# Kernel tuning notes

Hardware: AMD Instinct MI355X
Metric: run time of the kernel (lower is better)

The kernel has to match this reference:

```python
import jax, jax.numpy as jnp
import numpy as np

N = 50000        # nodes
E = 1_600_000    # edges
F_IN = 128       # in_channels
H = 128          # hidden_dim (== F_IN so GCN weights stack)
L = 3            # num_layers
LSTM_H = 256     # lstm_hidden
OUT = 32         # output_dim
G = 64           # number of graphs in the batch


def setup_inputs() -> dict:
    key = jax.random.key(0)
    ks = jax.random.split(key, 8)
    x = jax.random.normal(ks[0], (N, F_IN), dtype=jnp.float32)
    edge_index = jax.random.randint(ks[1], (2, E), 0, N, dtype=jnp.int32)
    batch = jnp.sort(jax.random.randint(ks[2], (N,), 0, G, dtype=jnp.int32))
    # GCN layer weights (all [H,H] since F_IN == H), PyG-style glorot scale
    Wg = jax.random.normal(ks[3], (L, F_IN, H), dtype=jnp.float32) / np.sqrt(F_IN)
    bg = jnp.zeros((L, H), dtype=jnp.float32)
    # torch LSTM params, gate order (i, f, g, o)
    W_ih = jax.random.normal(ks[4], (4 * LSTM_H, H), dtype=jnp.float32) / np.sqrt(H)
    W_hh = jax.random.normal(ks[5], (4 * LSTM_H, LSTM_H), dtype=jnp.float32) / np.sqrt(LSTM_H)
    b_ih = jnp.zeros((4 * LSTM_H,), dtype=jnp.float32)
    b_hh = jnp.zeros((4 * LSTM_H,), dtype=jnp.float32)
    W_out = jax.random.normal(ks[6], (OUT, LSTM_H), dtype=jnp.float32) / np.sqrt(LSTM_H)
    b_out = jnp.zeros((OUT,), dtype=jnp.float32)
    return dict(x=x, edge_index=edge_index, batch=batch, Wg=Wg, bg=bg,
                W_ih=W_ih, W_hh=W_hh, b_ih=b_ih, b_hh=b_hh,
                W_out=W_out, b_out=b_out)


def reference(x, edge_index, batch, Wg, bg, W_ih, W_hh, b_ih, b_hh, W_out, b_out):
    n = x.shape[0]
    # PyG GCNConv gcn_norm: add self-loops, symmetric D^{-1/2}(A+I)D^{-1/2}
    loop = jnp.arange(n, dtype=edge_index.dtype)
    row = jnp.concatenate([edge_index[0], loop])  # source nodes (x_j)
    col = jnp.concatenate([edge_index[1], loop])  # target nodes (aggregate here)
    deg = jax.ops.segment_sum(jnp.ones_like(col, dtype=x.dtype), col, num_segments=n)
    dinv = jnp.where(deg > 0, jax.lax.rsqrt(deg), 0.0)
    norm = (dinv[row] * dinv[col])[:, None]  # [E+N, 1]

    h = x
    for l in range(Wg.shape[0]):
        t = h @ Wg[l]                                     # [N, H] transform first
        msg = t[row] * norm                               # gather + scale  [E+N, H]
        agg = jax.ops.segment_sum(msg, col, num_segments=n)  # scatter-add  [N, H]
        h = jax.nn.relu(agg + bg[l])

    # global_mean_pool over batch segment ids
    cnt = jax.ops.segment_sum(jnp.ones((n,), h.dtype), batch, num_segments=G)
    pooled = jax.ops.segment_sum(h, batch, num_segments=G) / jnp.maximum(cnt, 1.0)[:, None]  # [G, H]

    # single-step LSTM with zero initial state (seq_len = 1)
    h0 = jnp.zeros((G, W_hh.shape[1]), pooled.dtype)
    gates = pooled @ W_ih.T + h0 @ W_hh.T + b_ih + b_hh   # [G, 4*LSTM_H]
    i, f, g, o = jnp.split(gates, 4, axis=-1)             # torch gate order i,f,g,o
    c = jax.nn.sigmoid(i) * jnp.tanh(g)                   # c0 = 0 => forget term drops
    hn = jax.nn.sigmoid(o) * jnp.tanh(c)                  # [G, LSTM_H]

    return hn @ W_out.T + b_out                            # [G, OUT]
```

## Files before the change

### kernel.cpp

```cpp
#include <hip/hip_runtime.h>

constexpr int NN = 50000;
constexpr int NE = 1600000;
constexpr int H  = 128;
constexpr int LH = 256;
constexpr int OD = 32;
constexpr int NG = 64;

constexpr int NBKT  = (NN + 255) / 256;
constexpr int PARTE = 4096;
constexpr int NPARTB = (NE + PARTE - 1) / PARTE;
static_assert(NBKT <= 256, "single-block scan assumes NBKT <= 256");

constexpr int BCH = 4;
constexpr int BCW = 32;

constexpr int LSZ = 4608;

typedef __attribute__((ext_vector_type(8))) short short8v;
typedef __attribute__((ext_vector_type(4))) float f32x4;

union BF8 { uint4 u; short8v s; };

__device__ __forceinline__ unsigned short f2bf(float x) {
    unsigned int u = __float_as_uint(x);
    u = (u + 0x7FFFu + ((u >> 16) & 1u)) >> 16;
    return (unsigned short)u;
}

__global__ __launch_bounds__(256) void k_bhist(const int* __restrict__ col,
                                               int* __restrict__ bktCnt) {
    __shared__ int h[NBKT];
    int t = threadIdx.x;
    if (t < NBKT) h[t] = 0;
    __syncthreads();
    for (int i = blockIdx.x * 256 + t; i < NE; i += gridDim.x * 256)
        atomicAdd(&h[col[i] >> 8], 1);
    __syncthreads();
    if (t < NBKT && h[t] > 0) atomicAdd(&bktCnt[t], h[t]);
}

__global__ __launch_bounds__(256) void k_bscan(const int* __restrict__ bktCnt,
                                               int* __restrict__ bktBase,
                                               int* __restrict__ bktCursor) {
    __shared__ int sh[256];
    int t = threadIdx.x;
    int v = (t < NBKT) ? bktCnt[t] : 0;
    sh[t] = v;
    __syncthreads();
    for (int off = 1; off < 256; off <<= 1) {
        int add = (t >= off) ? sh[t - off] : 0;
        __syncthreads();
        sh[t] += add;
        __syncthreads();
    }
    if (t < NBKT) {
        int excl = sh[t] - v;
        bktBase[t] = excl;
        bktCursor[t] = excl;
    }
    if (t == NBKT - 1) bktBase[NBKT] = sh[t];
}

__global__ __launch_bounds__(256) void k_part(const int* __restrict__ ei,
                                              int* __restrict__ bktCursor,
                                              int* __restrict__ part) {
    __shared__ int lcur[NBKT];
    __shared__ int lbase[NBKT];
    const int t = threadIdx.x;
    const int base = blockIdx.x * PARTE;
    int pk[16], bk[16];

    if (t < NBKT) lcur[t] = 0;
    __syncthreads();
#pragma unroll
    for (int j = 0; j < 16; ++j) {
        int e = base + j * 256 + t;
        if (e < NE) {
            int sr = ei[e];
            int ds = ei[NE + e];
            pk[j] = (sr << 8) | (ds & 255);
            bk[j] = ds >> 8;
            atomicAdd(&lcur[bk[j]], 1);
        }
    }
    __syncthreads();
    if (t < NBKT) {
        int c = lcur[t];
        lbase[t] = (c > 0) ? atomicAdd(&bktCursor[t], c) : 0;
        lcur[t] = 0;
    }
    __syncthreads();
#pragma unroll
    for (int j = 0; j < 16; ++j) {
        int e = base + j * 256 + t;
        if (e < NE) {
            int r = atomicAdd(&lcur[bk[j]], 1);
            part[lbase[bk[j]] + r] = pk[j];
        }
    }
}

__global__ __launch_bounds__(256) void k_bfill(const int* __restrict__ bktBase,
                                               const int* __restrict__ part,
                                               int* __restrict__ rp,
                                               int* __restrict__ cnt,
                                               float* __restrict__ dinv,
                                               int* __restrict__ srcs) {
    __shared__ int h[256];
    __shared__ int sc[256];
    __shared__ int cur[256];
    const int b = blockIdx.x, t = threadIdx.x;
    const int lo = bktBase[b], hi = bktBase[b + 1];

    h[t] = 0;
    __syncthreads();
    for (int i = lo + t; i < hi; i += 256)
        atomicAdd(&h[part[i] & 255], 1);
    __syncthreads();
    int v = h[t];
    sc[t] = v;
    __syncthreads();
    for (int off = 1; off < 256; off <<= 1) {
        int add = (t >= off) ? sc[t - off] : 0;
        __syncthreads();
        sc[t] += add;
        __syncthreads();
    }
    int excl = sc[t] - v;
    cur[t] = lo + excl;
    int node = b * 256 + t;
    if (node < NN) {
        rp[node] = lo + excl;
        cnt[node] = v;
        dinv[node] = rsqrtf((float)v + 1.0f);
    }
    __syncthreads();
    for (int i = lo + t; i < hi; i += 256) {
        int e = part[i];
        int pos = atomicAdd(&cur[e & 255], 1);
        srcs[pos] = e >> 8;
    }
}

template <bool RELU, bool CHIN>
__global__ __launch_bounds__(256) void k_gemm(const float* __restrict__ hf,
                                              const unsigned short* __restrict__ hb,
                                              const float* __restrict__ W,
                                              const float* __restrict__ dinv,
                                              unsigned short* __restrict__ tb) {
    __shared__ uint4 lw[2048];
    const int tid = threadIdx.x;

    for (int e = tid; e < 2048; e += 256) {
        const int ct = e >> 8, ks = (e >> 6) & 3, l = e & 63;
        const int col = ct * 16 + (l & 15);
        const int kb  = ks * 32 + ((l >> 4) << 3);
        const float* wp = W + (size_t)kb * H + col;
        unsigned int p0 = (unsigned)f2bf(wp[0])     | ((unsigned)f2bf(wp[H])     << 16);
        unsigned int p1 = (unsigned)f2bf(wp[2 * H]) | ((unsigned)f2bf(wp[3 * H]) << 16);
        unsigned int p2 = (unsigned)f2bf(wp[4 * H]) | ((unsigned)f2bf(wp[5 * H]) << 16);
        unsigned int p3 = (unsigned)f2bf(wp[6 * H]) | ((unsigned)f2bf(wp[7 * H]) << 16);
        lw[e] = make_uint4(p0, p1, p2, p3);
    }
    __syncthreads();

    const int wave = tid >> 6, lane = tid & 63;
    const int rowbase = blockIdx.x * 64 + wave * 16;
    const int arow  = rowbase + (lane & 15);
    const int arowc = arow < NN ? arow : NN - 1;
    const int koff  = (lane >> 4) << 3;

    f32x4 acc[8];
#pragma unroll
    for (int ct = 0; ct < 8; ++ct) acc[ct] = (f32x4){0.f, 0.f, 0.f, 0.f};

#pragma unroll
    for (int ks = 0; ks < 4; ++ks) {
        BF8 a;
        if (CHIN) {
            a.u = *reinterpret_cast<const uint4*>(
                hb + ((size_t)ks * NN + arowc) * BCW + koff);
            if (RELU) {
                unsigned int m;
                m = ((a.u.x >> 15) & 0x00010001u) * 0xFFFFu; a.u.x &= ~m;
                m = ((a.u.y >> 15) & 0x00010001u) * 0xFFFFu; a.u.y &= ~m;
                m = ((a.u.z >> 15) & 0x00010001u) * 0xFFFFu; a.u.z &= ~m;
                m = ((a.u.w >> 15) & 0x00010001u) * 0xFFFFu; a.u.w &= ~m;
            }
        } else {
            const int kb = ks * 32 + koff;
            const float* base = hf + (size_t)arowc * H + kb;
            float4 h0 = *reinterpret_cast<const float4*>(base);
            float4 h1 = *reinterpret_cast<const float4*>(base + 4);
            if (RELU) {
                h0.x = fmaxf(h0.x, 0.f); h0.y = fmaxf(h0.y, 0.f);
                h0.z = fmaxf(h0.z, 0.f); h0.w = fmaxf(h0.w, 0.f);
                h1.x = fmaxf(h1.x, 0.f); h1.y = fmaxf(h1.y, 0.f);
                h1.z = fmaxf(h1.z, 0.f); h1.w = fmaxf(h1.w, 0.f);
            }
            a.u = make_uint4(
                (unsigned)f2bf(h0.x) | ((unsigned)f2bf(h0.y) << 16),
                (unsigned)f2bf(h0.z) | ((unsigned)f2bf(h0.w) << 16),
                (unsigned)f2bf(h1.x) | ((unsigned)f2bf(h1.y) << 16),
                (unsigned)f2bf(h1.z) | ((unsigned)f2bf(h1.w) << 16));
        }
#pragma unroll
        for (int ct = 0; ct < 8; ++ct) {
            BF8 b;
            b.u = lw[(ct * 4 + ks) * 64 + lane];
            acc[ct] = __builtin_amdgcn_mfma_f32_16x16x32_bf16(a.s, b.s, acc[ct], 0, 0, 0);
        }
    }

    const int colb = lane & 15;
    const int rrow = rowbase + ((lane >> 4) << 2);
#pragma unroll
    for (int r = 0; r < 4; ++r) {
        const int row = rrow + r;
        if (row < NN) {
            const float d = dinv[row];
#pragma unroll
            for (int ct = 0; ct < 8; ++ct) {
                const int feat = ct * 16 + colb;
                tb[((size_t)(feat >> 5) * NN + row) * BCW + (feat & 31)] =
                    f2bf(acc[ct][r] * d);
            }
        }
    }
}

template <int POOL>
__global__ __launch_bounds__(256) void k_gather(const int* __restrict__ rp,
                                                const int* __restrict__ cnt,
                                                const int* __restrict__ srcs,
                                                const float* __restrict__ dinv,
                                                const float* __restrict__ bg,
                                                const unsigned short* __restrict__ tb,
                                                unsigned short* __restrict__ aggb,
                                                const int* __restrict__ batch,
                                                float* __restrict__ pooled) {
    __shared__ int lsrcs[LSZ];
    const int tid  = threadIdx.x;
    const int wv   = tid >> 6;
    const int lane = tid & 63;
    const int slot = lane >> 2;
    const int l4   = lane & 3;
    const int c    = blockIdx.x & 3;
    const int nb   = blockIdx.x >> 2;
    const int n0   = nb * 64;
    const int n    = n0 + wv * 16 + slot;

    const int eLo = rp[n0];
    int nLast = n0 + 63; if (nLast >= NN) nLast = NN - 1;
    const int eHi = rp[nLast] + cnt[nLast];
    const bool staged = (eHi - eLo) <= LSZ;

    if (staged) {
        for (int i = eLo + tid; i < eHi; i += 256)
            lsrcs[i - eLo] = srcs[i];
    }

    __shared__ float psum[4][32];
    int g0 = 0, gspan = 0;
    if (POOL) {
        if (tid < 128) psum[tid >> 5][tid & 31] = 0.f;
        g0 = batch[n0];
        gspan = batch[nLast] - g0;
    }
    __syncthreads();

    if (n >= NN) return;

    const uint4* __restrict__ tb4 =
        reinterpret_cast<const uint4*>(tb) + (size_t)c * NN * 4;
    const float4 bg0 = *reinterpret_cast<const float4*>(bg + c * BCW + l4 * 8);
    const float4 bg1 = *reinterpret_cast<const float4*>(bg + c * BCW + l4 * 8 + 4);

    const int i0  = rp[n];
    const int end = i0 + cnt[n];
    float4 p = make_float4(0.f, 0.f, 0.f, 0.f);
    float4 q = make_float4(0.f, 0.f, 0.f, 0.f);

#define ACC8(v)                                                        \
    do {                                                               \
        p.x += __uint_as_float((v).x << 16);                           \
        p.y += __uint_as_float((v).x & 0xFFFF0000u);                   \
        p.z += __uint_as_float((v).y << 16);                           \
        p.w += __uint_as_float((v).y & 0xFFFF0000u);                   \
        q.x += __uint_as_float((v).z << 16);                           \
        q.y += __uint_as_float((v).z & 0xFFFF0000u);                   \
        q.z += __uint_as_float((v).w << 16);                           \
        q.w += __uint_as_float((v).w & 0xFFFF0000u);                   \
    } while (0)

    if (staged) {
        int i = i0;
        for (; i + 7 < end; i += 8) {
            int s0 = lsrcs[i     - eLo], s1 = lsrcs[i + 1 - eLo];
            int s2 = lsrcs[i + 2 - eLo], s3 = lsrcs[i + 3 - eLo];
            int s4 = lsrcs[i + 4 - eLo], s5 = lsrcs[i + 5 - eLo];
            int s6 = lsrcs[i + 6 - eLo], s7 = lsrcs[i + 7 - eLo];
            uint4 v0 = tb4[(size_t)s0 * 4 + l4];
            uint4 v1 = tb4[(size_t)s1 * 4 + l4];
            uint4 v2 = tb4[(size_t)s2 * 4 + l4];
            uint4 v3 = tb4[(size_t)s3 * 4 + l4];
            uint4 v4 = tb4[(size_t)s4 * 4 + l4];
            uint4 v5 = tb4[(size_t)s5 * 4 + l4];
            uint4 v6 = tb4[(size_t)s6 * 4 + l4];
            uint4 v7 = tb4[(size_t)s7 * 4 + l4];
            ACC8(v0); ACC8(v1); ACC8(v2); ACC8(v3);
            ACC8(v4); ACC8(v5); ACC8(v6); ACC8(v7);
        }
        for (; i < end; ++i) {
            uint4 v = tb4[(size_t)lsrcs[i - eLo] * 4 + l4];
            ACC8(v);
        }
    } else {
        int i = i0;
        for (; i + 3 < end; i += 4) {
            int s0 = srcs[i], s1 = srcs[i + 1], s2 = srcs[i + 2], s3 = srcs[i + 3];
            uint4 v0 = tb4[(size_t)s0 * 4 + l4];
            uint4 v1 = tb4[(size_t)s1 * 4 + l4];
            uint4 v2 = tb4[(size_t)s2 * 4 + l4];
            uint4 v3 = tb4[(size_t)s3 * 4 + l4];
            ACC8(v0); ACC8(v1); ACC8(v2); ACC8(v3);
        }
        for (; i < end; ++i) {
            uint4 v = tb4[(size_t)srcs[i] * 4 + l4];
            ACC8(v);
        }
    }

    uint4 sv = tb4[(size_t)n * 4 + l4];
    ACC8(sv);
#undef ACC8

    const float d = dinv[n];
    float4 o0, o1;
    o0.x = fmaf(p.x, d, bg0.x); o0.y = fmaf(p.y, d, bg0.y);
    o0.z = fmaf(p.z, d, bg0.z); o0.w = fmaf(p.w, d, bg0.w);
    o1.x = fmaf(q.x, d, bg1.x); o1.y = fmaf(q.y, d, bg1.y);
    o1.z = fmaf(q.z, d, bg1.z); o1.w = fmaf(q.w, d, bg1.w);

    if (POOL == 0) {
        uint4 u;
        u.x = (unsigned)f2bf(o0.x) | ((unsigned)f2bf(o0.y) << 16);
        u.y = (unsigned)f2bf(o0.z) | ((unsigned)f2bf(o0.w) << 16);
        u.z = (unsigned)f2bf(o1.x) | ((unsigned)f2bf(o1.y) << 16);
        u.w = (unsigned)f2bf(o1.z) | ((unsigned)f2bf(o1.w) << 16);
        *reinterpret_cast<uint4*>(aggb + ((size_t)c * NN + n) * BCW + l4 * 8) = u;
    } else {
        o0.x = fmaxf(o0.x, 0.f); o0.y = fmaxf(o0.y, 0.f);
        o0.z = fmaxf(o0.z, 0.f); o0.w = fmaxf(o0.w, 0.f);
        o1.x = fmaxf(o1.x, 0.f); o1.y = fmaxf(o1.y, 0.f);
        o1.z = fmaxf(o1.z, 0.f); o1.w = fmaxf(o1.w, 0.f);
        if (gspan > 3) {
            float* dst = pooled + (size_t)batch[n] * H + c * BCW + l4 * 8;
            atomicAdd(dst + 0, o0.x); atomicAdd(dst + 1, o0.y);
            atomicAdd(dst + 2, o0.z); atomicAdd(dst + 3, o0.w);
            atomicAdd(dst + 4, o1.x); atomicAdd(dst + 5, o1.y);
            atomicAdd(dst + 6, o1.z); atomicAdd(dst + 7, o1.w);
        } else if (gspan == 0) {
#pragma unroll
            for (int m = 4; m <= 32; m <<= 1) {
                o0.x += __shfl_xor(o0.x, m); o0.y += __shfl_xor(o0.y, m);
                o0.z += __shfl_xor(o0.z, m); o0.w += __shfl_xor(o0.w, m);
                o1.x += __shfl_xor(o1.x, m); o1.y += __shfl_xor(o1.y, m);
                o1.z += __shfl_xor(o1.z, m); o1.w += __shfl_xor(o1.w, m);
            }
            if (slot == 0) {
                float* ps = &psum[wv][l4 * 8];
                ps[0] = o0.x; ps[1] = o0.y; ps[2] = o0.z; ps[3] = o0.w;
                ps[4] = o1.x; ps[5] = o1.y; ps[6] = o1.z; ps[7] = o1.w;
            }
            __syncthreads();
            if (tid < 32) {
                float v = psum[0][tid] + psum[1][tid] + psum[2][tid] + psum[3][tid];
                atomicAdd(&pooled[(size_t)g0 * H + c * BCW + tid], v);
            }
        } else {
            const int gi = batch[n] - g0;
            float* ps = &psum[gi][l4 * 8];
            atomicAdd(ps + 0, o0.x); atomicAdd(ps + 1, o0.y);
            atomicAdd(ps + 2, o0.z); atomicAdd(ps + 3, o0.w);
            atomicAdd(ps + 4, o1.x); atomicAdd(ps + 5, o1.y);
            atomicAdd(ps + 6, o1.z); atomicAdd(ps + 7, o1.w);
            __syncthreads();
            if (tid < 128) {
                int gi2 = tid >> 5, f = tid & 31;
                float v = psum[gi2][f];
                if (v != 0.f)
                    atomicAdd(&pooled[(size_t)(g0 + gi2) * H + c * BCW + f], v);
            }
        }
    }
}

__device__ __forceinline__ int lower_bound_dev(const int* __restrict__ b, int v) {
    int lo = 0, hi = NN;
    while (lo < hi) {
        int m = (lo + hi) >> 1;
        if (b[m] < v) lo = m + 1; else hi = m;
    }
    return lo;
}

__global__ __launch_bounds__(256) void k_lstm(const float* __restrict__ pooled,
                                              const int* __restrict__ batch,
                                              const float* __restrict__ W_ih,
                                              const float* __restrict__ b_ih,
                                              const float* __restrict__ b_hh,
                                              const float* __restrict__ W_out,
                                              const float* __restrict__ b_out,
                                              float* __restrict__ out) {
    __shared__ __align__(16) float p[H];
    __shared__ __align__(16) float hn[LH];
    int g = blockIdx.x, t = threadIdx.x;
    if (t < H) {
        int s = lower_bound_dev(batch, g);
        int e = lower_bound_dev(batch, g + 1);
        p[t] = pooled[g * H + t] / fmaxf((float)(e - s), 1.f);
    }
    __syncthreads();

    float si = b_ih[t] + b_hh[t];
    float sg = b_ih[2 * LH + t] + b_hh[2 * LH + t];
    float so = b_ih[3 * LH + t] + b_hh[3 * LH + t];
    const float* wi = W_ih + (size_t)t * H;
    const float* wg = W_ih + (size_t)(2 * LH + t) * H;
    const float* wo = W_ih + (size_t)(3 * LH + t) * H;
    for (int k = 0; k < H; k += 4) {
        float4 pv = *reinterpret_cast<const float4*>(&p[k]);
        float4 a = *reinterpret_cast<const float4*>(wi + k);
        si += pv.x * a.x + pv.y * a.y + pv.z * a.z + pv.w * a.w;
        float4 b = *reinterpret_cast<const float4*>(wg + k);
        sg += pv.x * b.x + pv.y * b.y + pv.z * b.z + pv.w * b.w;
        float4 c = *reinterpret_cast<const float4*>(wo + k);
        so += pv.x * c.x + pv.y * c.y + pv.z * c.z + pv.w * c.w;
    }
    float ig = 1.f / (1.f + expf(-si));
    float cc = ig * tanhf(sg);
    float og = 1.f / (1.f + expf(-so));
    hn[t] = og * tanhf(cc);
    __syncthreads();

    if (t < OD) {
        float acc = b_out[t];
        const float* wr = W_out + (size_t)t * LH;
        for (int k = 0; k < LH; k += 4) {
            float4 hv = *reinterpret_cast<const float4*>(&hn[k]);
            float4 wv = *reinterpret_cast<const float4*>(wr + k);
            acc += hv.x * wv.x + hv.y * wv.y + hv.z * wv.z + hv.w * wv.w;
        }
        out[g * OD + t] = acc;
    }
}

extern "C" void kernel_launch(void* const* d_in, const int* in_sizes, int n_in,
                              void* d_out, int out_size, void* d_ws, size_t ws_size,
                              hipStream_t stream) {
    const float* x     = (const float*)d_in[0];
    const int*   ei    = (const int*)d_in[1];
    const int*   batch = (const int*)d_in[2];
    const float* Wg    = (const float*)d_in[3];
    const float* bg    = (const float*)d_in[4];
    const float* W_ih  = (const float*)d_in[5];
    const float* b_ih  = (const float*)d_in[7];
    const float* b_hh  = (const float*)d_in[8];
    const float* W_out = (const float*)d_in[9];
    const float* b_out = (const float*)d_in[10];
    float* out = (float*)d_out;

    unsigned short* tb   = (unsigned short*)d_ws;
    unsigned short* aggb = tb + (size_t)NN * H;
    int*   part      = (int*)(aggb + (size_t)NN * H);
    float* dinv      = (float*)(part + NE);
    float* pooled    = dinv + NN;
    int*   cnt       = (int*)(pooled + NG * H);
    int*   rp        = cnt + NN;
    int*   srcs      = rp + NN;
    int*   bktCnt    = srcs + NE;
    int*   bktBase   = bktCnt + NBKT;
    int*   bktCursor = bktBase + NBKT + 1;

    hipMemsetAsync(bktCnt, 0, NBKT * sizeof(int), stream);
    hipMemsetAsync(pooled, 0, NG * H * sizeof(float), stream);

    k_bhist<<<256, 256, 0, stream>>>(ei + NE, bktCnt);
    k_bscan<<<1, 256, 0, stream>>>(bktCnt, bktBase, bktCursor);
    k_part <<<NPARTB, 256, 0, stream>>>(ei, bktCursor, part);
    k_bfill<<<NBKT, 256, 0, stream>>>(bktBase, part, rp, cnt, dinv, srcs);

    const int gemmBlocks = (NN + 63) / 64;
    const int gathBlocks = ((NN + 63) / 64) * BCH;

    k_gemm<false, false><<<gemmBlocks, 256, 0, stream>>>(x, nullptr, Wg, dinv, tb);
    k_gather<0><<<gathBlocks, 256, 0, stream>>>(rp, cnt, srcs, dinv, bg, tb, aggb, batch, pooled);
    k_gemm<true, true><<<gemmBlocks, 256, 0, stream>>>(nullptr, aggb, Wg + H * H, dinv, tb);
    k_gather<0><<<gathBlocks, 256, 0, stream>>>(rp, cnt, srcs, dinv, bg + H, tb, aggb, batch, pooled);
    k_gemm<true, true><<<gemmBlocks, 256, 0, stream>>>(nullptr, aggb, Wg + 2 * H * H, dinv, tb);
    k_gather<1><<<gathBlocks, 256, 0, stream>>>(rp, cnt, srcs, dinv, bg + 2 * H, tb, nullptr, batch, pooled);

    k_lstm<<<NG, 256, 0, stream>>>(pooled, batch, W_ih, b_ih, b_hh, W_out, b_out, out);
}
```

Before: 261.4 us.

## Compress edge sources to 16-bit, pad gather loops with zero row, finer buckets

Stores the CSR source indices as unsigned short instead of int, which halves index traffic in the gather kernels. The bf16 feature buffers gain a padding row that is set to zero, so the gather loops can round each degree up to a multiple of 8 and drop their scalar tail loops. The non-staged path is also widened to 8 gathers per iteration. Bucket width in the CSR build drops from 256 to 128 nodes and the histogram grid grows. The catch is that a 16-bit index cannot hold node ids of 65536 or more, so correctness depends on N=50000, and the k_bfill store (e >> 7) keeps only 16 bits.

```diff
diff --git a/kernel.cpp b/kernel.cpp
--- a/kernel.cpp
+++ b/kernel.cpp
@@ -7,13 +7,14 @@
 constexpr int OD = 32;
 constexpr int NG = 64;
 
-constexpr int NBKT  = (NN + 255) / 256;
+constexpr int NBKT  = (NN + 127) / 128;
 constexpr int PARTE = 4096;
 constexpr int NPARTB = (NE + PARTE - 1) / PARTE;
-static_assert(NBKT <= 256, "single-block scan assumes NBKT <= 256");
+static_assert(NBKT <= 512, "k_bscan single block of 512 assumes NBKT <= 512");
 
 constexpr int BCH = 4;
 constexpr int BCW = 32;
+constexpr int NNP = NN + 1;
 
 constexpr int LSZ = 4608;
 
@@ -28,27 +29,33 @@
     return (unsigned short)u;
 }
 
+__global__ __launch_bounds__(128) void k_zrow(unsigned short* __restrict__ tb) {
+    int t = threadIdx.x;
+    tb[((size_t)(t >> 5) * NNP + NN) * BCW + (t & 31)] = 0;
+}
+
 __global__ __launch_bounds__(256) void k_bhist(const int* __restrict__ col,
                                                int* __restrict__ bktCnt) {
     __shared__ int h[NBKT];
     int t = threadIdx.x;
-    if (t < NBKT) h[t] = 0;
+    for (int i = t; i < NBKT; i += 256) h[i] = 0;
     __syncthreads();
     for (int i = blockIdx.x * 256 + t; i < NE; i += gridDim.x * 256)
-        atomicAdd(&h[col[i] >> 8], 1);
-    __syncthreads();
-    if (t < NBKT && h[t] > 0) atomicAdd(&bktCnt[t], h[t]);
-}
-
-__global__ __launch_bounds__(256) void k_bscan(const int* __restrict__ bktCnt,
+        atomicAdd(&h[col[i] >> 7], 1);
+    __syncthreads();
+    for (int i = t; i < NBKT; i += 256)
+        if (h[i] > 0) atomicAdd(&bktCnt[i], h[i]);
+}
+
+__global__ __launch_bounds__(512) void k_bscan(const int* __restrict__ bktCnt,
                                                int* __restrict__ bktBase,
                                                int* __restrict__ bktCursor) {
-    __shared__ int sh[256];
+    __shared__ int sh[512];
     int t = threadIdx.x;
     int v = (t < NBKT) ? bktCnt[t] : 0;
     sh[t] = v;
     __syncthreads();
-    for (int off = 1; off < 256; off <<= 1) {
+    for (int off = 1; off < 512; off <<= 1) {
         int add = (t >= off) ? sh[t - off] : 0;
         __syncthreads();
         sh[t] += add;
@@ -71,7 +78,7 @@
     const int base = blockIdx.x * PARTE;
     int pk[16], bk[16];
 
-    if (t < NBKT) lcur[t] = 0;
+    for (int i = t; i < NBKT; i += 256) lcur[i] = 0;
     __syncthreads();
 #pragma unroll
     for (int j = 0; j < 16; ++j) {
@@ -79,16 +86,16 @@
         if (e < NE) {
             int sr = ei[e];
             int ds = ei[NE + e];
-            pk[j] = (sr << 8) | (ds & 255);
-            bk[j] = ds >> 8;
+            pk[j] = (sr << 7) | (ds & 127);
+            bk[j] = ds >> 7;
             atomicAdd(&lcur[bk[j]], 1);
         }
     }
     __syncthreads();
-    if (t < NBKT) {
-        int c = lcur[t];
-        lbase[t] = (c > 0) ? atomicAdd(&bktCursor[t], c) : 0;
-        lcur[t] = 0;
+    for (int i = t; i < NBKT; i += 256) {
+        int c = lcur[i];
+        lbase[i] = (c > 0) ? atomicAdd(&bktCursor[i], c) : 0;
+        lcur[i] = 0;
     }
     __syncthreads();
 #pragma unroll
@@ -106,40 +113,43 @@
                                                int* __restrict__ rp,
                                                int* __restrict__ cnt,
                                                float* __restrict__ dinv,
-                                               int* __restrict__ srcs) {
-    __shared__ int h[256];
-    __shared__ int sc[256];
-    __shared__ int cur[256];
+                                               unsigned short* __restrict__ srcs) {
+    __shared__ int h[128];
+    __shared__ int sc[128];
+    __shared__ int cur[128];
     const int b = blockIdx.x, t = threadIdx.x;
     const int lo = bktBase[b], hi = bktBase[b + 1];
 
-    h[t] = 0;
+    if (t < 128) h[t] = 0;
     __syncthreads();
     for (int i = lo + t; i < hi; i += 256)
-        atomicAdd(&h[part[i] & 255], 1);
-    __syncthreads();
-    int v = h[t];
-    sc[t] = v;
-    __syncthreads();
-    for (int off = 1; off < 256; off <<= 1) {
-        int add = (t >= off) ? sc[t - off] : 0;
+        atomicAdd(&h[part[i] & 127], 1);
+    __syncthreads();
+    int v = 0;
+    if (t < 128) { v = h[t]; sc[t] = v; }
+    __syncthreads();
+    for (int off = 1; off < 128; off <<= 1) {
+        int add = 0;
+        if (t < 128 && t >= off) add = sc[t - off];
         __syncthreads();
-        sc[t] += add;
+        if (t < 128) sc[t] += add;
         __syncthreads();
     }
-    int excl = sc[t] - v;
-    cur[t] = lo + excl;
-    int node = b * 256 + t;
-    if (node < NN) {
-        rp[node] = lo + excl;
-        cnt[node] = v;
-        dinv[node] = rsqrtf((float)v + 1.0f);
+    if (t < 128) {
+        int excl = sc[t] - v;
+        cur[t] = lo + excl;
+        int node = b * 128 + t;
+        if (node < NN) {
+            rp[node] = lo + excl;
+            cnt[node] = v;
+            dinv[node] = rsqrtf((float)v + 1.0f);
+        }
     }
     __syncthreads();
     for (int i = lo + t; i < hi; i += 256) {
         int e = part[i];
-        int pos = atomicAdd(&cur[e & 255], 1);
-        srcs[pos] = e >> 8;
+        int pos = atomicAdd(&cur[e & 127], 1);
+        srcs[pos] = (unsigned short)(e >> 7);
     }
 }
 
@@ -180,7 +190,7 @@
         BF8 a;
         if (CHIN) {
             a.u = *reinterpret_cast<const uint4*>(
-                hb + ((size_t)ks * NN + arowc) * BCW + koff);
+                hb + ((size_t)ks * NNP + arowc) * BCW + koff);
             if (RELU) {
                 unsigned int m;
                 m = ((a.u.x >> 15) & 0x00010001u) * 0xFFFFu; a.u.x &= ~m;
@@ -223,7 +233,7 @@
 #pragma unroll
             for (int ct = 0; ct < 8; ++ct) {
                 const int feat = ct * 16 + colb;
-                tb[((size_t)(feat >> 5) * NN + row) * BCW + (feat & 31)] =
+                tb[((size_t)(feat >> 5) * NNP + row) * BCW + (feat & 31)] =
                     f2bf(acc[ct][r] * d);
             }
         }
@@ -233,14 +243,14 @@
 template <int POOL>
 __global__ __launch_bounds__(256) void k_gather(const int* __restrict__ rp,
                                                 const int* __restrict__ cnt,
-                                                const int* __restrict__ srcs,
+                                                const unsigned short* __restrict__ srcs,
                                                 const float* __restrict__ dinv,
                                                 const float* __restrict__ bg,
                                                 const unsigned short* __restrict__ tb,
                                                 unsigned short* __restrict__ aggb,
                                                 const int* __restrict__ batch,
                                                 float* __restrict__ pooled) {
-    __shared__ int lsrcs[LSZ];
+    __shared__ unsigned short lsrcs[LSZ + 8];
     const int tid  = threadIdx.x;
     const int wv   = tid >> 6;
     const int lane = tid & 63;
@@ -273,12 +283,14 @@
     if (n >= NN) return;
 
     const uint4* __restrict__ tb4 =
-        reinterpret_cast<const uint4*>(tb) + (size_t)c * NN * 4;
+        reinterpret_cast<const uint4*>(tb) + (size_t)c * NNP * 4;
     const float4 bg0 = *reinterpret_cast<const float4*>(bg + c * BCW + l4 * 8);
     const float4 bg1 = *reinterpret_cast<const float4*>(bg + c * BCW + l4 * 8 + 4);
 
-    const int i0  = rp[n];
-    const int end = i0 + cnt[n];
+    const int i0   = rp[n];
+    const int deg  = cnt[n];
+    const int end  = i0 + deg;
+    const int endP = i0 + ((deg + 7) & ~7);
     float4 p = make_float4(0.f, 0.f, 0.f, 0.f);
     float4 q = make_float4(0.f, 0.f, 0.f, 0.f);
 
@@ -295,12 +307,16 @@
     } while (0)
 
     if (staged) {
-        int i = i0;
-        for (; i + 7 < end; i += 8) {
-            int s0 = lsrcs[i     - eLo], s1 = lsrcs[i + 1 - eLo];
-            int s2 = lsrcs[i + 2 - eLo], s3 = lsrcs[i + 3 - eLo];
-            int s4 = lsrcs[i + 4 - eLo], s5 = lsrcs[i + 5 - eLo];
-            int s6 = lsrcs[i + 6 - eLo], s7 = lsrcs[i + 7 - eLo];
+        for (int i = i0; i < endP; i += 8) {
+            const int j = i - eLo;
+            int s0 = (i + 0 < end) ? (int)lsrcs[j + 0] : NN;
+            int s1 = (i + 1 < end) ? (int)lsrcs[j + 1] : NN;
+            int s2 = (i + 2 < end) ? (int)lsrcs[j + 2] : NN;
+            int s3 = (i + 3 < end) ? (int)lsrcs[j + 3] : NN;
+            int s4 = (i + 4 < end) ? (int)lsrcs[j + 4] : NN;
+            int s5 = (i + 5 < end) ? (int)lsrcs[j + 5] : NN;
+            int s6 = (i + 6 < end) ? (int)lsrcs[j + 6] : NN;
+            int s7 = (i + 7 < end) ? (int)lsrcs[j + 7] : NN;
             uint4 v0 = tb4[(size_t)s0 * 4 + l4];
             uint4 v1 = tb4[(size_t)s1 * 4 + l4];
             uint4 v2 = tb4[(size_t)s2 * 4 + l4];
@@ -312,23 +328,26 @@
             ACC8(v0); ACC8(v1); ACC8(v2); ACC8(v3);
             ACC8(v4); ACC8(v5); ACC8(v6); ACC8(v7);
         }
-        for (; i < end; ++i) {
-            uint4 v = tb4[(size_t)lsrcs[i - eLo] * 4 + l4];
-            ACC8(v);
-        }
     } else {
-        int i = i0;
-        for (; i + 3 < end; i += 4) {
-            int s0 = srcs[i], s1 = srcs[i + 1], s2 = srcs[i + 2], s3 = srcs[i + 3];
+        for (int i = i0; i < endP; i += 8) {
+            int s0 = (i + 0 < end) ? (int)srcs[i + 0] : NN;
+            int s1 = (i + 1 < end) ? (int)srcs[i + 1] : NN;
+            int s2 = (i + 2 < end) ? (int)srcs[i + 2] : NN;
+            int s3 = (i + 3 < end) ? (int)srcs[i + 3] : NN;
+            int s4 = (i + 4 < end) ? (int)srcs[i + 4] : NN;
+            int s5 = (i + 5 < end) ? (int)srcs[i + 5] : NN;
+            int s6 = (i + 6 < end) ? (int)srcs[i + 6] : NN;
+            int s7 = (i + 7 < end) ? (int)srcs[i + 7] : NN;
             uint4 v0 = tb4[(size_t)s0 * 4 + l4];
             uint4 v1 = tb4[(size_t)s1 * 4 + l4];
             uint4 v2 = tb4[(size_t)s2 * 4 + l4];
             uint4 v3 = tb4[(size_t)s3 * 4 + l4];
+            uint4 v4 = tb4[(size_t)s4 * 4 + l4];
+            uint4 v5 = tb4[(size_t)s5 * 4 + l4];
+            uint4 v6 = tb4[(size_t)s6 * 4 + l4];
+            uint4 v7 = tb4[(size_t)s7 * 4 + l4];
             ACC8(v0); ACC8(v1); ACC8(v2); ACC8(v3);
-        }
-        for (; i < end; ++i) {
-            uint4 v = tb4[(size_t)srcs[i] * 4 + l4];
-            ACC8(v);
+            ACC8(v4); ACC8(v5); ACC8(v6); ACC8(v7);
         }
     }
 
@@ -349,7 +368,7 @@
         u.y = (unsigned)f2bf(o0.z) | ((unsigned)f2bf(o0.w) << 16);
         u.z = (unsigned)f2bf(o1.x) | ((unsigned)f2bf(o1.y) << 16);
         u.w = (unsigned)f2bf(o1.z) | ((unsigned)f2bf(o1.w) << 16);
-        *reinterpret_cast<uint4*>(aggb + ((size_t)c * NN + n) * BCW + l4 * 8) = u;
+        *reinterpret_cast<uint4*>(aggb + ((size_t)c * NNP + n) * BCW + l4 * 8) = u;
     } else {
         o0.x = fmaxf(o0.x, 0.f); o0.y = fmaxf(o0.y, 0.f);
         o0.z = fmaxf(o0.z, 0.f); o0.w = fmaxf(o0.w, 0.f);
@@ -473,22 +492,23 @@
     float* out = (float*)d_out;
 
     unsigned short* tb   = (unsigned short*)d_ws;
-    unsigned short* aggb = tb + (size_t)NN * H;
-    int*   part      = (int*)(aggb + (size_t)NN * H);
+    unsigned short* aggb = tb + (size_t)4 * NNP * BCW;
+    int*   part      = (int*)(aggb + (size_t)4 * NNP * BCW);
     float* dinv      = (float*)(part + NE);
     float* pooled    = dinv + NN;
     int*   cnt       = (int*)(pooled + NG * H);
     int*   rp        = cnt + NN;
-    int*   srcs      = rp + NN;
-    int*   bktCnt    = srcs + NE;
+    unsigned short* srcs = (unsigned short*)(rp + NN);
+    int*   bktCnt    = (int*)(srcs + NE + 16);
     int*   bktBase   = bktCnt + NBKT;
     int*   bktCursor = bktBase + NBKT + 1;
 
     hipMemsetAsync(bktCnt, 0, NBKT * sizeof(int), stream);
     hipMemsetAsync(pooled, 0, NG * H * sizeof(float), stream);
-
-    k_bhist<<<256, 256, 0, stream>>>(ei + NE, bktCnt);
-    k_bscan<<<1, 256, 0, stream>>>(bktCnt, bktBase, bktCursor);
+    k_zrow<<<1, 128, 0, stream>>>(tb);
+
+    k_bhist<<<1024, 256, 0, stream>>>(ei + NE, bktCnt);
+    k_bscan<<<1, 512, 0, stream>>>(bktCnt, bktBase, bktCursor);
     k_part <<<NPARTB, 256, 0, stream>>>(ei, bktCursor, part);
     k_bfill<<<NBKT, 256, 0, stream>>>(bktBase, part, rp, cnt, dinv, srcs);
 
```

After: 276.5 us. +5.8%, slower.
